# Performance work log

Hardware: AMD Instinct MI355X
Metric: run time of the kernel (lower is better)

Reference implementation:

```python
import jax, jax.numpy as jnp
import numpy as np

N_OBJ, IN_DIM, MID_DIM, OUT_DIM = 2048, 128, 256, 1


def setup_inputs() -> dict:
    key = jax.random.key(0)
    ks = jax.random.split(key, 7)
    s = 0.05  # keep sigmoid inputs in a sane range
    return {
        "x": jax.random.normal(ks[0], (N_OBJ, IN_DIM), dtype=jnp.float32),
        "W1": jax.random.normal(ks[1], (N_OBJ, MID_DIM, IN_DIM), dtype=jnp.float32) * s,
        "b1": jax.random.normal(ks[2], (N_OBJ, MID_DIM), dtype=jnp.float32) * s,
        "W2": jax.random.normal(ks[3], (N_OBJ, MID_DIM, MID_DIM), dtype=jnp.float32) * s,
        "b2": jax.random.normal(ks[4], (N_OBJ, MID_DIM), dtype=jnp.float32) * s,
        "W3": jax.random.normal(ks[5], (N_OBJ, OUT_DIM, MID_DIM), dtype=jnp.float32) * s,
        "b3": jax.random.normal(ks[6], (N_OBJ, OUT_DIM), dtype=jnp.float32) * s,
    }


def reference(x, W1, b1, W2, b2, W3, b3):
    # Per-object 3-layer MLP, batched as grouped GEMV over the object axis.
    # NOTE: faithful to original — NO activation after fc1.
    y1 = jnp.einsum("oi,omi->om", x, W1) + b1            # [O, mid]
    y2 = jax.nn.sigmoid(jnp.einsum("om,onm->on", y1, W2) + b2)  # [O, mid]
    y3 = jax.nn.sigmoid(jnp.einsum("on,okn->ok", y2, W3) + b3)  # [O, 1]
    return y3[:, 0]  # [n_objects]
```

## Files before the change

### kernel.cpp

```cpp
#include <hip/hip_runtime.h>
#include <math.h>


#define N_OBJ   2048
#define IN_DIM  128
#define MID_DIM 256

__global__ __launch_bounds__(256, 8) void mlp_grouped_kernel(
    const float* __restrict__ x,
    const float* __restrict__ W1,
    const float* __restrict__ b1,
    const float* __restrict__ W2,
    const float* __restrict__ b2,
    const float* __restrict__ W3,
    const float* __restrict__ b3,
    float* __restrict__ out)
{
    const int o = blockIdx.x;
    const int t = threadIdx.x;

    __shared__ __align__(16) float s_x[IN_DIM];
    __shared__ __align__(16) float s_y1[MID_DIM];
    __shared__ __align__(16) float s_y2[MID_DIM];
    __shared__ float s_red[4];

    if (t < IN_DIM) s_x[t] = x[(size_t)o * IN_DIM + t];
    __syncthreads();

    {
        const float4* w = (const float4*)(W1 + (size_t)o * MID_DIM * IN_DIM
                                             + (size_t)t * IN_DIM);
        const float4* xv = (const float4*)s_x;
        float acc = 0.0f;
        #pragma unroll 8
        for (int j = 0; j < IN_DIM / 4; ++j) {
            float4 wv = w[j];
            float4 v  = xv[j];
            acc += wv.x * v.x + wv.y * v.y + wv.z * v.z + wv.w * v.w;
        }
        s_y1[t] = acc + b1[(size_t)o * MID_DIM + t];
    }
    __syncthreads();

    {
        const float4* w = (const float4*)(W2 + (size_t)o * MID_DIM * MID_DIM
                                             + (size_t)t * MID_DIM);
        const float4* yv = (const float4*)s_y1;
        float acc = 0.0f;
        #pragma unroll 8
        for (int j = 0; j < MID_DIM / 4; ++j) {
            float4 wv = w[j];
            float4 v  = yv[j];
            acc += wv.x * v.x + wv.y * v.y + wv.z * v.z + wv.w * v.w;
        }
        acc += b2[(size_t)o * MID_DIM + t];
        s_y2[t] = 1.0f / (1.0f + expf(-acc));
    }
    __syncthreads();

    {
        float p = s_y2[t] * W3[(size_t)o * MID_DIM + t];
        #pragma unroll
        for (int off = 32; off > 0; off >>= 1)
            p += __shfl_down(p, off, 64);
        if ((t & 63) == 0) s_red[t >> 6] = p;
        __syncthreads();
        if (t == 0) {
            float s = s_red[0] + s_red[1] + s_red[2] + s_red[3]
                    + b3[o];
            out[o] = 1.0f / (1.0f + expf(-s));
        }
    }
}

extern "C" void kernel_launch(void* const* d_in, const int* in_sizes, int n_in,
                              void* d_out, int out_size, void* d_ws, size_t ws_size,
                              hipStream_t stream) {
    const float* x  = (const float*)d_in[0];
    const float* W1 = (const float*)d_in[1];
    const float* b1 = (const float*)d_in[2];
    const float* W2 = (const float*)d_in[3];
    const float* b2 = (const float*)d_in[4];
    const float* W3 = (const float*)d_in[5];
    const float* b3 = (const float*)d_in[6];
    float* out = (float*)d_out;

    mlp_grouped_kernel<<<N_OBJ, 256, 0, stream>>>(x, W1, b1, W2, b2, W3, b3, out);
}
```

Measured before the change: 836.9 us.

## Use wave-per-row coalesced weight loads with shuffle reductions for GEMV layers

Each wavefront now handles 64 output rows: its lanes load one contiguous row of W1/W2 together, so the loads are fully coalesced, and the partial dot products are combined with a cross-lane shuffle reduction. Previously each thread walked its own row with a large stride between lanes. This targets the global-memory access pattern of a memory-bound weight stream, at the cost of one 6-step shuffle reduction per output row. The x load into shared memory is also vectorized to float4.

After: 857.4 us. 2.5% more time.

```diff
diff --git a/kernel.cpp b/kernel.cpp
--- a/kernel.cpp
+++ b/kernel.cpp
@@ -18,43 +18,50 @@
 {
     const int o = blockIdx.x;
     const int t = threadIdx.x;
+    const int w = t >> 6;
+    const int l = t & 63;
 
     __shared__ __align__(16) float s_x[IN_DIM];
     __shared__ __align__(16) float s_y1[MID_DIM];
     __shared__ __align__(16) float s_y2[MID_DIM];
     __shared__ float s_red[4];
 
-    if (t < IN_DIM) s_x[t] = x[(size_t)o * IN_DIM + t];
+    if (t < IN_DIM / 4)
+        ((float4*)s_x)[t] = ((const float4*)(x + (size_t)o * IN_DIM))[t];
     __syncthreads();
 
     {
-        const float4* w = (const float4*)(W1 + (size_t)o * MID_DIM * IN_DIM
-                                             + (size_t)t * IN_DIM);
-        const float4* xv = (const float4*)s_x;
-        float acc = 0.0f;
-        #pragma unroll 8
-        for (int j = 0; j < IN_DIM / 4; ++j) {
-            float4 wv = w[j];
-            float4 v  = xv[j];
-            acc += wv.x * v.x + wv.y * v.y + wv.z * v.z + wv.w * v.w;
+        const float* W1o = W1 + (size_t)o * MID_DIM * IN_DIM;
+        const float2 xv = ((const float2*)s_x)[l];
+        #pragma unroll 4
+        for (int i = 0; i < 64; ++i) {
+            const int r = w * 64 + i;
+            float2 wv = ((const float2*)(W1o + (size_t)r * IN_DIM))[l];
+            float p = wv.x * xv.x + wv.y * xv.y;
+            #pragma unroll
+            for (int off = 32; off > 0; off >>= 1)
+                p += __shfl_down(p, off, 64);
+            if (l == 0) s_y1[r] = p + b1[(size_t)o * MID_DIM + r];
         }
-        s_y1[t] = acc + b1[(size_t)o * MID_DIM + t];
     }
     __syncthreads();
 
     {
-        const float4* w = (const float4*)(W2 + (size_t)o * MID_DIM * MID_DIM
-                                             + (size_t)t * MID_DIM);
-        const float4* yv = (const float4*)s_y1;
-        float acc = 0.0f;
-        #pragma unroll 8
-        for (int j = 0; j < MID_DIM / 4; ++j) {
-            float4 wv = w[j];
-            float4 v  = yv[j];
-            acc += wv.x * v.x + wv.y * v.y + wv.z * v.z + wv.w * v.w;
+        const float* W2o = W2 + (size_t)o * MID_DIM * MID_DIM;
+        const float4 yv = ((const float4*)s_y1)[l];
+        #pragma unroll 4
+        for (int i = 0; i < 64; ++i) {
+            const int r = w * 64 + i;
+            float4 wv = ((const float4*)(W2o + (size_t)r * MID_DIM))[l];
+            float p = wv.x * yv.x + wv.y * yv.y + wv.z * yv.z + wv.w * yv.w;
+            #pragma unroll
+            for (int off = 32; off > 0; off >>= 1)
+                p += __shfl_down(p, off, 64);
+            if (l == 0) {
+                float a = p + b2[(size_t)o * MID_DIM + r];
+                s_y2[r] = 1.0f / (1.0f + expf(-a));
+            }
         }
-        acc += b2[(size_t)o * MID_DIM + t];
-        s_y2[t] = 1.0f / (1.0f + expf(-acc));
     }
     __syncthreads();
 
@@ -63,11 +70,10 @@
         #pragma unroll
         for (int off = 32; off > 0; off >>= 1)
             p += __shfl_down(p, off, 64);
-        if ((t & 63) == 0) s_red[t >> 6] = p;
+        if (l == 0) s_red[w] = p;
         __syncthreads();
         if (t == 0) {
-            float s = s_red[0] + s_red[1] + s_red[2] + s_red[3]
-                    + b3[o];
+            float s = s_red[0] + s_red[1] + s_red[2] + s_red[3] + b3[o];
             out[o] = 1.0f / (1.0f + expf(-s));
         }
     }
```
